# Kernel optimization log

Measured on AMD Instinct MI355X. Metric: run time of the kernel, lower is better.

Reference implementation:

```python
import jax, jax.numpy as jnp
import numpy as np

NUM_HEADS = 16


def setup_inputs() -> dict:
    key = jax.random.key(0)
    ks = jax.random.split(key, 8)
    B, S, D = 2, 2048, 1024
    q = jax.random.normal(ks[0], (B, S, D), dtype=jnp.float32)
    k = jax.random.normal(ks[1], (B, S, D), dtype=jnp.float32)
    v = jax.random.normal(ks[2], (B, S, D), dtype=jnp.float32)
    mask = jax.random.randint(ks[3], (1, 1, S, S), 0, 2, dtype=jnp.int32)
    sc = 1.0 / np.sqrt(D)
    wq = jax.random.normal(ks[4], (D, D), dtype=jnp.float32) * sc
    wk = jax.random.normal(ks[5], (D, D), dtype=jnp.float32) * sc
    wv = jax.random.normal(ks[6], (D, D), dtype=jnp.float32) * sc
    wout = jax.random.normal(ks[7], (D, D), dtype=jnp.float32) * sc
    return {"q": q, "k": k, "v": v, "mask": mask,
            "wq": wq, "wk": wk, "wv": wv, "wout": wout}


def reference(q, k, v, mask, wq, wk, wv, wout):
    B, S, D = q.shape
    H = NUM_HEADS
    hd = D // H

    def proj(x, w):
        # nn.Linear(bias=False): x @ w.T, then split heads -> [B,H,S,hd]
        return (x @ w.T).reshape(B, -1, H, hd).transpose(0, 2, 1, 3)

    qh, kh, vh = proj(q, wq), proj(k, wk), proj(v, wv)
    scale = jnp.asarray(hd, q.dtype) ** 0.5
    scores = jnp.einsum('bhqd,bhkd->bhqk', qh, kh) / scale  # [B,H,S,S]
    att = jax.nn.softmax(scores, axis=-1)
    # NOTE: original applies masked_fill AFTER softmax with value -1e-9
    att = jnp.where(mask == 0, jnp.asarray(-1e-9, att.dtype), att)
    out = jnp.einsum('bhqk,bhkd->bhqd', att, vh)  # [B,H,S,hd]
    out = out.transpose(0, 2, 1, 3).reshape(B, S, D)
    return out @ wout.T
```

## Files before the change

### kernel.cpp

```cpp
#include <hip/hip_runtime.h>
#include <stdint.h>


#define BATCH  2
#define S_LEN  2048
#define DMODEL 1024
#define NH     16
#define HD     64

typedef __bf16 bf16_t;
typedef short  short8 __attribute__((ext_vector_type(8)));
typedef float  f32x4  __attribute__((ext_vector_type(4)));

#define AS1 __attribute__((address_space(1)))
#define AS3 __attribute__((address_space(3)))

static constexpr size_t MB = (size_t)1 << 20;
static constexpr size_t WS_REQUIRED = 112 * MB;
#define OFF_XHI(z)  ((size_t)(z) * 16 * MB)
#define OFF_XLO(z)  (OFF_XHI(z) + 8 * MB)
#define OFF_WHI(z)  (48 * MB + (size_t)(z) * 4 * MB)
#define OFF_WLO(z)  (OFF_WHI(z) + 2 * MB)
#define OFF_PHI(z)  (64 * MB + (size_t)(z) * 16 * MB)
#define OFF_PLO(z)  (OFF_PHI(z) + 8 * MB)
#define OFF_OHI     ((size_t)0)
#define OFF_OLO     (8 * MB)
#define OFF_MASKB   (16 * MB)

__device__ __forceinline__ f32x4 mfma_bf16(short8 a, short8 b, f32x4 c) {
    return __builtin_amdgcn_mfma_f32_16x16x32_bf16(a, b, c, 0, 0, 0);
}

__device__ __forceinline__ short8 ld8(const bf16_t* p) {
    return *reinterpret_cast<const short8*>(p);
}

__global__ void cvt_split_kernel(const float* __restrict__ x,
                                 bf16_t* __restrict__ hi, bf16_t* __restrict__ lo,
                                 int n) {
    int i = (blockIdx.x * blockDim.x + threadIdx.x) * 4;
    if (i >= n) return;
    const float4 v = *reinterpret_cast<const float4*>(x + i);
    float s[4] = {v.x, v.y, v.z, v.w};
    ushort hbits[4], lbits[4];
#pragma unroll
    for (int j = 0; j < 4; j++) {
        bf16_t hh = (bf16_t)s[j];
        bf16_t ll = (bf16_t)(s[j] - (float)hh);
        hbits[j] = __builtin_bit_cast(ushort, hh);
        lbits[j] = __builtin_bit_cast(ushort, ll);
    }
    *reinterpret_cast<ushort4*>(hi + i) = ushort4{hbits[0], hbits[1], hbits[2], hbits[3]};
    *reinterpret_cast<ushort4*>(lo + i) = ushort4{lbits[0], lbits[1], lbits[2], lbits[3]};
}

__global__ void cvt_mask_kernel(const int* __restrict__ m, bf16_t* __restrict__ mb, int n) {
    int i = (blockIdx.x * blockDim.x + threadIdx.x) * 4;
    if (i >= n) return;
    const int4 v = *reinterpret_cast<const int4*>(m + i);
    int s[4] = {v.x, v.y, v.z, v.w};
    ushort b[4];
#pragma unroll
    for (int j = 0; j < 4; j++) {
        bf16_t t = (bf16_t)(s[j] ? 1.0f : 0.0f);
        b[j] = __builtin_bit_cast(ushort, t);
    }
    *reinterpret_cast<ushort4*>(mb + i) = ushort4{b[0], b[1], b[2], b[3]};
}

template <int FINAL>
__global__ __launch_bounds__(256, 2) void gemm_split_kernel(char* __restrict__ ws,
                                                            float* __restrict__ fout) {
    __shared__ __align__(16) bf16_t As[128 * 32];
    __shared__ __align__(16) bf16_t Bs[128 * 32];

    const int z = FINAL ? 3 : blockIdx.z;
    const bf16_t* Ahi = FINAL ? (const bf16_t*)(ws + OFF_OHI) : (const bf16_t*)(ws + OFF_XHI(z));
    const bf16_t* Alo = FINAL ? (const bf16_t*)(ws + OFF_OLO) : (const bf16_t*)(ws + OFF_XLO(z));
    const bf16_t* Bhi = (const bf16_t*)(ws + OFF_WHI(z));
    const bf16_t* Blo = (const bf16_t*)(ws + OFF_WLO(z));
    bf16_t* Ohi = FINAL ? nullptr : (bf16_t*)(ws + OFF_PHI(z));
    bf16_t* Olo = FINAL ? nullptr : (bf16_t*)(ws + OFF_PLO(z));
    const float scale = (!FINAL && z == 0) ? 0.125f : 1.0f;

    const int tid = threadIdx.x;
    const int lane = tid & 63, w = tid >> 6;
    const int wr = w >> 1, wc = w & 1;
    const int fr = lane & 15, fg = lane >> 4;
    const int m0 = blockIdx.x * 128, n0 = blockIdx.y * 128;
    const int K = 1024;

    const bf16_t* Aseg[3] = {Ahi, Ahi, Alo};
    const bf16_t* Bseg[3] = {Bhi, Blo, Bhi};

    f32x4 acc[4][4];
#pragma unroll
    for (int i = 0; i < 4; i++)
#pragma unroll
        for (int j = 0; j < 4; j++) acc[i][j] = f32x4{0.f, 0.f, 0.f, 0.f};

    AS3 bf16_t* asA = (AS3 bf16_t*)As;
    AS3 bf16_t* asB = (AS3 bf16_t*)Bs;

#pragma unroll 1
    for (int seg = 0; seg < 3; ++seg) {
        const bf16_t* Ab = Aseg[seg];
        const bf16_t* Bb = Bseg[seg];
#pragma unroll 1
        for (int ks = 0; ks < K; ks += 32) {
            __syncthreads();
#pragma unroll
            for (int i = 0; i < 2; i++) {
                const int c = i * 256 + tid;
                const int row = c >> 2;
                const int ce = (c & 3) * 8;
                __builtin_amdgcn_global_load_lds((const AS1 void*)(Ab + (size_t)(m0 + row) * K + ks + ce),
                                                 (AS3 void*)(asA + (size_t)(i * 256 + w * 64) * 8),
                                                 16, 0, 0);
                __builtin_amdgcn_global_load_lds((const AS1 void*)(Bb + (size_t)(n0 + row) * K + ks + ce),
                                                 (AS3 void*)(asB + (size_t)(i * 256 + w * 64) * 8),
                                                 16, 0, 0);
            }
            __syncthreads();

            short8 af[4], bfr[4];
#pragma unroll
            for (int i = 0; i < 4; i++) {
                af[i]  = ld8(&As[(wr * 64 + i * 16 + fr) * 32 + fg * 8]);
                bfr[i] = ld8(&Bs[(wc * 64 + i * 16 + fr) * 32 + fg * 8]);
            }
#pragma unroll
            for (int i = 0; i < 4; i++)
#pragma unroll
                for (int j = 0; j < 4; j++)
                    acc[i][j] = mfma_bf16(af[i], bfr[j], acc[i][j]);
        }
    }

#pragma unroll
    for (int i = 0; i < 4; i++) {
#pragma unroll
        for (int j = 0; j < 4; j++) {
            const int ncol = n0 + wc * 64 + j * 16 + fr;
#pragma unroll
            for (int r = 0; r < 4; r++) {
                const int m = m0 + wr * 64 + i * 16 + fg * 4 + r;
                const float val = acc[i][j][r] * scale;
                if (FINAL) {
                    fout[(size_t)m * DMODEL + ncol] = val;
                } else {
                    const bf16_t h = (bf16_t)val;
                    const bf16_t l = (bf16_t)(val - (float)h);
                    const int b = m >> 11, s = m & (S_LEN - 1);
                    const int hh = ncol >> 6, d = ncol & (HD - 1);
                    size_t idx;
                    if (z == 2) idx = ((size_t)(b * NH + hh) * HD + d) * S_LEN + s;
                    else        idx = ((size_t)(b * NH + hh) * S_LEN + s) * HD + d;
                    Ohi[idx] = h;
                    Olo[idx] = l;
                }
            }
        }
    }
}

__global__ __launch_bounds__(256, 2) void attn_kernel(char* __restrict__ ws) {
    __shared__ __align__(16) bf16_t KsH[8 * 64 * 8];
    __shared__ __align__(16) bf16_t KsL[8 * 64 * 8];
    __shared__ __align__(16) bf16_t VsH[8 * 64 * 8];
    __shared__ __align__(16) bf16_t VsL[8 * 64 * 8];

    const bf16_t* Qhi = (const bf16_t*)(ws + OFF_PHI(0));
    const bf16_t* Qlo = (const bf16_t*)(ws + OFF_PLO(0));
    const bf16_t* Khi = (const bf16_t*)(ws + OFF_PHI(1));
    const bf16_t* Klo = (const bf16_t*)(ws + OFF_PLO(1));
    const bf16_t* Vhi = (const bf16_t*)(ws + OFF_PHI(2));
    const bf16_t* Vlo = (const bf16_t*)(ws + OFF_PLO(2));
    const bf16_t* Mb  = (const bf16_t*)(ws + OFF_MASKB);
    bf16_t* Ohi = (bf16_t*)(ws + OFF_OHI);
    bf16_t* Olo = (bf16_t*)(ws + OFF_OLO);

    const int tid = threadIdx.x, lane = tid & 63, w = tid >> 6;
    const int fr = lane & 15, fg = lane >> 4;
    const int bh = blockIdx.y;
    const int q0 = blockIdx.x * 64;
    const int qrow = q0 + w * 16 + fr;
    const size_t qkBase = (size_t)bh * S_LEN * HD;
    const size_t vtBase = (size_t)bh * HD * S_LEN;

    size_t kSrc[2], vSrc[2];
#pragma unroll
    for (int i = 0; i < 2; i++) {
        const int s = i * 256 + tid;
        const int l = s & 63, f = (s >> 6) & 7;
        const int sfr = l & 15, sfg = l >> 4;
        const int cf = f >> 1, kc = f & 1;
        const int r = (cf & 1) * 4 + (sfr & 3) + (sfr >> 2) * 8 + (cf >> 1) * 32;
        kSrc[i] = qkBase + (size_t)r * HD + kc * 32 + sfg * 8;
        vSrc[i] = vtBase + (size_t)((f >> 1) * 16 + sfr) * S_LEN + (f & 1) * 32 + sfg * 8;
    }

    AS3 bf16_t* asKH = (AS3 bf16_t*)KsH;
    AS3 bf16_t* asKL = (AS3 bf16_t*)KsL;
    AS3 bf16_t* asVH = (AS3 bf16_t*)VsH;
    AS3 bf16_t* asVL = (AS3 bf16_t*)VsL;

    short8 qh[2], ql[2];
#pragma unroll
    for (int kc = 0; kc < 2; kc++) {
        const size_t off = qkBase + (size_t)qrow * HD + kc * 32 + fg * 8;
        qh[kc] = ld8(Qhi + off);
        ql[kc] = ld8(Qlo + off);
    }

    f32x4 acco[4];
#pragma unroll
    for (int df = 0; df < 4; df++) acco[df] = f32x4{0.f, 0.f, 0.f, 0.f};
    float mrun = -__builtin_inff(), lrun = 0.f;

    const size_t mrowBase = (size_t)qrow * S_LEN;

#pragma unroll 1
    for (int k0 = 0; k0 < S_LEN; k0 += 64) {
        __syncthreads();
#pragma unroll
        for (int i = 0; i < 2; i++) {
            const size_t ko = kSrc[i] + (size_t)k0 * HD;
            const size_t vo = vSrc[i] + k0;
            const size_t dst = (size_t)(i * 256 + w * 64) * 8;
            __builtin_amdgcn_global_load_lds((const AS1 void*)(Khi + ko), (AS3 void*)(asKH + dst), 16, 0, 0);
            __builtin_amdgcn_global_load_lds((const AS1 void*)(Klo + ko), (AS3 void*)(asKL + dst), 16, 0, 0);
            __builtin_amdgcn_global_load_lds((const AS1 void*)(Vhi + vo), (AS3 void*)(asVH + dst), 16, 0, 0);
            __builtin_amdgcn_global_load_lds((const AS1 void*)(Vlo + vo), (AS3 void*)(asVL + dst), 16, 0, 0);
        }
        const short8 mv0 = ld8(Mb + mrowBase + k0 + fg * 8);
        const short8 mv1 = ld8(Mb + mrowBase + k0 + 32 + fg * 8);
        __syncthreads();

        f32x4 sacc[4];
#pragma unroll
        for (int cf = 0; cf < 4; cf++) sacc[cf] = f32x4{0.f, 0.f, 0.f, 0.f};
#pragma unroll
        for (int cf = 0; cf < 4; cf++) {
#pragma unroll
            for (int kc = 0; kc < 2; kc++) {
                const int fi = cf * 2 + kc;
                const short8 kh = ld8(&KsH[(fi * 64 + lane) * 8]);
                const short8 kl = ld8(&KsL[(fi * 64 + lane) * 8]);
                sacc[cf] = mfma_bf16(kh, qh[kc], sacc[cf]);
                sacc[cf] = mfma_bf16(kl, qh[kc], sacc[cf]);
                sacc[cf] = mfma_bf16(kh, ql[kc], sacc[cf]);
            }
        }

        float mx = sacc[0][0];
#pragma unroll
        for (int cf = 0; cf < 4; cf++)
#pragma unroll
            for (int r = 0; r < 4; r++) mx = fmaxf(mx, sacc[cf][r]);
        mx = fmaxf(mx, __shfl_xor(mx, 16, 64));
        mx = fmaxf(mx, __shfl_xor(mx, 32, 64));
        const float mnew = fmaxf(mrun, mx);
        const float alpha = __expf(mrun - mnew);
        mrun = mnew;

        float p[4][4], psum = 0.f;
#pragma unroll
        for (int cf = 0; cf < 4; cf++)
#pragma unroll
            for (int r = 0; r < 4; r++) {
                p[cf][r] = __expf(sacc[cf][r] - mnew);
                psum += p[cf][r];
            }
        psum += __shfl_xor(psum, 16, 64);
        psum += __shfl_xor(psum, 32, 64);
        lrun = lrun * alpha + psum;
#pragma unroll
        for (int df = 0; df < 4; df++) acco[df] *= alpha;

        short8 phi[2], plo[2];
#pragma unroll
        for (int kc2 = 0; kc2 < 2; kc2++) {
#pragma unroll
            for (int j = 0; j < 8; j++) {
                const int cf = kc2 * 2 + (j >> 2), r = j & 3;
                const float mvf = (float)__builtin_bit_cast(
                    bf16_t, (ushort)((cf >> 1) ? mv1[(cf & 1) * 4 + r] : mv0[(cf & 1) * 4 + r]));
                const float pm = p[cf][r] * mvf;
                const bf16_t h = (bf16_t)pm;
                const bf16_t l = (bf16_t)(pm - (float)h);
                phi[kc2][j] = __builtin_bit_cast(short, h);
                plo[kc2][j] = __builtin_bit_cast(short, l);
            }
        }

#pragma unroll
        for (int kc2 = 0; kc2 < 2; kc2++) {
#pragma unroll
            for (int df = 0; df < 4; df++) {
                const int fi = df * 2 + kc2;
                const short8 vh = ld8(&VsH[(fi * 64 + lane) * 8]);
                const short8 vl = ld8(&VsL[(fi * 64 + lane) * 8]);
                acco[df] = mfma_bf16(vh, phi[kc2], acco[df]);
                acco[df] = mfma_bf16(vl, phi[kc2], acco[df]);
                acco[df] = mfma_bf16(vh, plo[kc2], acco[df]);
            }
        }
    }

    const int b = bh >> 4, hh = bh & (NH - 1);
    const float inv = 1.0f / lrun;
    const size_t obase = ((size_t)b * S_LEN + qrow) * DMODEL + hh * HD;
#pragma unroll
    for (int df = 0; df < 4; df++) {
#pragma unroll
        for (int r = 0; r < 4; r++) {
            const int d = df * 16 + fg * 4 + r;
            const float o = acco[df][r] * inv;
            const bf16_t h = (bf16_t)o;
            Ohi[obase + d] = h;
            Olo[obase + d] = (bf16_t)(o - (float)h);
        }
    }
}

extern "C" void kernel_launch(void* const* d_in, const int* in_sizes, int n_in,
                              void* d_out, int out_size, void* d_ws, size_t ws_size,
                              hipStream_t stream) {
    (void)in_sizes; (void)n_in; (void)out_size;
    if (ws_size < WS_REQUIRED) return;

    const float* q    = (const float*)d_in[0];
    const float* k    = (const float*)d_in[1];
    const float* v    = (const float*)d_in[2];
    const int*   mask = (const int*)  d_in[3];
    const float* wq   = (const float*)d_in[4];
    const float* wk   = (const float*)d_in[5];
    const float* wv   = (const float*)d_in[6];
    const float* wout = (const float*)d_in[7];
    char* ws = (char*)d_ws;
    float* out = (float*)d_out;

    const size_t nX = (size_t)BATCH * S_LEN * DMODEL;
    const size_t nW = (size_t)DMODEL * DMODEL;
    const size_t nM = (size_t)S_LEN * S_LEN;
    const dim3 blk(256);

    cvt_split_kernel<<<dim3(nX / 1024), blk, 0, stream>>>(q, (bf16_t*)(ws + OFF_XHI(0)), (bf16_t*)(ws + OFF_XLO(0)), (int)nX);
    cvt_split_kernel<<<dim3(nX / 1024), blk, 0, stream>>>(k, (bf16_t*)(ws + OFF_XHI(1)), (bf16_t*)(ws + OFF_XLO(1)), (int)nX);
    cvt_split_kernel<<<dim3(nX / 1024), blk, 0, stream>>>(v, (bf16_t*)(ws + OFF_XHI(2)), (bf16_t*)(ws + OFF_XLO(2)), (int)nX);
    cvt_split_kernel<<<dim3(nW / 1024), blk, 0, stream>>>(wq,   (bf16_t*)(ws + OFF_WHI(0)), (bf16_t*)(ws + OFF_WLO(0)), (int)nW);
    cvt_split_kernel<<<dim3(nW / 1024), blk, 0, stream>>>(wk,   (bf16_t*)(ws + OFF_WHI(1)), (bf16_t*)(ws + OFF_WLO(1)), (int)nW);
    cvt_split_kernel<<<dim3(nW / 1024), blk, 0, stream>>>(wv,   (bf16_t*)(ws + OFF_WHI(2)), (bf16_t*)(ws + OFF_WLO(2)), (int)nW);
    cvt_split_kernel<<<dim3(nW / 1024), blk, 0, stream>>>(wout, (bf16_t*)(ws + OFF_WHI(3)), (bf16_t*)(ws + OFF_WLO(3)), (int)nW);

    gemm_split_kernel<0><<<dim3(32, 8, 3), blk, 0, stream>>>(ws, nullptr);

    cvt_mask_kernel<<<dim3(nM / 1024), blk, 0, stream>>>(mask, (bf16_t*)(ws + OFF_MASKB), (int)nM);

    attn_kernel<<<dim3(S_LEN / 64, BATCH * NH), blk, 0, stream>>>(ws);

    gemm_split_kernel<1><<<dim3(32, 8, 1), blk, 0, stream>>>(ws, out);
}
```

Measured before the change: 485.6 us.

## Double-buffer attention K/V tiles and fuse split-bf16 GEMM segments

The attention kernel now double-buffers the K/V hi/lo tiles in LDS. It issues the next tile's async global-to-LDS loads and the next mask loads before computing on the current tile, with one barrier per iteration and s_setprio raised around the MFMA sections. The projection GEMM loads hi and lo tiles of both operands together and does all three split products in a single K loop, where it used to make three separate passes over K. This is meant to hide memory latency in attention and cut GEMM loop and barrier overhead and A/B reloads. The cost is double the LDS in both kernels, which may lower occupancy, plus more registers for the extra fragments.

```diff
diff --git a/kernel.cpp b/kernel.cpp
--- a/kernel.cpp
+++ b/kernel.cpp
@@ -71,8 +71,10 @@
 template <int FINAL>
 __global__ __launch_bounds__(256, 2) void gemm_split_kernel(char* __restrict__ ws,
                                                             float* __restrict__ fout) {
-    __shared__ __align__(16) bf16_t As[128 * 32];
-    __shared__ __align__(16) bf16_t Bs[128 * 32];
+    __shared__ __align__(16) bf16_t AsH[128 * 32];
+    __shared__ __align__(16) bf16_t AsL[128 * 32];
+    __shared__ __align__(16) bf16_t BsH[128 * 32];
+    __shared__ __align__(16) bf16_t BsL[128 * 32];
 
     const int z = FINAL ? 3 : blockIdx.z;
     const bf16_t* Ahi = FINAL ? (const bf16_t*)(ws + OFF_OHI) : (const bf16_t*)(ws + OFF_XHI(z));
@@ -90,51 +92,53 @@
     const int m0 = blockIdx.x * 128, n0 = blockIdx.y * 128;
     const int K = 1024;
 
-    const bf16_t* Aseg[3] = {Ahi, Ahi, Alo};
-    const bf16_t* Bseg[3] = {Bhi, Blo, Bhi};
-
     f32x4 acc[4][4];
 #pragma unroll
     for (int i = 0; i < 4; i++)
 #pragma unroll
         for (int j = 0; j < 4; j++) acc[i][j] = f32x4{0.f, 0.f, 0.f, 0.f};
 
-    AS3 bf16_t* asA = (AS3 bf16_t*)As;
-    AS3 bf16_t* asB = (AS3 bf16_t*)Bs;
+    AS3 bf16_t* asAH = (AS3 bf16_t*)AsH;
+    AS3 bf16_t* asAL = (AS3 bf16_t*)AsL;
+    AS3 bf16_t* asBH = (AS3 bf16_t*)BsH;
+    AS3 bf16_t* asBL = (AS3 bf16_t*)BsL;
 
 #pragma unroll 1
-    for (int seg = 0; seg < 3; ++seg) {
-        const bf16_t* Ab = Aseg[seg];
-        const bf16_t* Bb = Bseg[seg];
-#pragma unroll 1
-        for (int ks = 0; ks < K; ks += 32) {
-            __syncthreads();
-#pragma unroll
-            for (int i = 0; i < 2; i++) {
-                const int c = i * 256 + tid;
-                const int row = c >> 2;
-                const int ce = (c & 3) * 8;
-                __builtin_amdgcn_global_load_lds((const AS1 void*)(Ab + (size_t)(m0 + row) * K + ks + ce),
-                                                 (AS3 void*)(asA + (size_t)(i * 256 + w * 64) * 8),
-                                                 16, 0, 0);
-                __builtin_amdgcn_global_load_lds((const AS1 void*)(Bb + (size_t)(n0 + row) * K + ks + ce),
-                                                 (AS3 void*)(asB + (size_t)(i * 256 + w * 64) * 8),
-                                                 16, 0, 0);
-            }
-            __syncthreads();
-
-            short8 af[4], bfr[4];
-#pragma unroll
-            for (int i = 0; i < 4; i++) {
-                af[i]  = ld8(&As[(wr * 64 + i * 16 + fr) * 32 + fg * 8]);
-                bfr[i] = ld8(&Bs[(wc * 64 + i * 16 + fr) * 32 + fg * 8]);
-            }
-#pragma unroll
-            for (int i = 0; i < 4; i++)
-#pragma unroll
-                for (int j = 0; j < 4; j++)
-                    acc[i][j] = mfma_bf16(af[i], bfr[j], acc[i][j]);
-        }
+    for (int ks = 0; ks < K; ks += 32) {
+        __syncthreads();
+#pragma unroll
+        for (int i = 0; i < 2; i++) {
+            const int c = i * 256 + tid;
+            const int row = c >> 2;
+            const int ce = (c & 3) * 8;
+            const size_t gA = (size_t)(m0 + row) * K + ks + ce;
+            const size_t gB = (size_t)(n0 + row) * K + ks + ce;
+            const size_t d = (size_t)(i * 256 + w * 64) * 8;
+            __builtin_amdgcn_global_load_lds((const AS1 void*)(Ahi + gA), (AS3 void*)(asAH + d), 16, 0, 0);
+            __builtin_amdgcn_global_load_lds((const AS1 void*)(Alo + gA), (AS3 void*)(asAL + d), 16, 0, 0);
+            __builtin_amdgcn_global_load_lds((const AS1 void*)(Bhi + gB), (AS3 void*)(asBH + d), 16, 0, 0);
+            __builtin_amdgcn_global_load_lds((const AS1 void*)(Blo + gB), (AS3 void*)(asBL + d), 16, 0, 0);
+        }
+        __syncthreads();
+
+        short8 afh[4], afl[4], bfh[4], bfl[4];
+#pragma unroll
+        for (int i = 0; i < 4; i++) {
+            const int ao = (wr * 64 + i * 16 + fr) * 32 + fg * 8;
+            const int bo = (wc * 64 + i * 16 + fr) * 32 + fg * 8;
+            afh[i] = ld8(&AsH[ao]);
+            afl[i] = ld8(&AsL[ao]);
+            bfh[i] = ld8(&BsH[bo]);
+            bfl[i] = ld8(&BsL[bo]);
+        }
+#pragma unroll
+        for (int i = 0; i < 4; i++)
+#pragma unroll
+            for (int j = 0; j < 4; j++) {
+                acc[i][j] = mfma_bf16(afh[i], bfh[j], acc[i][j]);
+                acc[i][j] = mfma_bf16(afh[i], bfl[j], acc[i][j]);
+                acc[i][j] = mfma_bf16(afl[i], bfh[j], acc[i][j]);
+            }
     }
 
 #pragma unroll
@@ -165,10 +169,10 @@
 }
 
 __global__ __launch_bounds__(256, 2) void attn_kernel(char* __restrict__ ws) {
-    __shared__ __align__(16) bf16_t KsH[8 * 64 * 8];
-    __shared__ __align__(16) bf16_t KsL[8 * 64 * 8];
-    __shared__ __align__(16) bf16_t VsH[8 * 64 * 8];
-    __shared__ __align__(16) bf16_t VsL[8 * 64 * 8];
+    __shared__ __align__(16) bf16_t KsH[2][8 * 64 * 8];
+    __shared__ __align__(16) bf16_t KsL[2][8 * 64 * 8];
+    __shared__ __align__(16) bf16_t VsH[2][8 * 64 * 8];
+    __shared__ __align__(16) bf16_t VsL[2][8 * 64 * 8];
 
     const bf16_t* Qhi = (const bf16_t*)(ws + OFF_PHI(0));
     const bf16_t* Qlo = (const bf16_t*)(ws + OFF_PLO(0));
@@ -200,11 +204,6 @@
         vSrc[i] = vtBase + (size_t)((f >> 1) * 16 + sfr) * S_LEN + (f & 1) * 32 + sfg * 8;
     }
 
-    AS3 bf16_t* asKH = (AS3 bf16_t*)KsH;
-    AS3 bf16_t* asKL = (AS3 bf16_t*)KsL;
-    AS3 bf16_t* asVH = (AS3 bf16_t*)VsH;
-    AS3 bf16_t* asVL = (AS3 bf16_t*)VsL;
-
     short8 qh[2], ql[2];
 #pragma unroll
     for (int kc = 0; kc < 2; kc++) {
@@ -220,38 +219,55 @@
 
     const size_t mrowBase = (size_t)qrow * S_LEN;
 
+#define STAGE(K0, BUF)                                                                             \
+    {                                                                                              \
+        _Pragma("unroll") for (int i = 0; i < 2; i++) {                                            \
+            const size_t ko = kSrc[i] + (size_t)(K0) * HD;                                         \
+            const size_t vo = vSrc[i] + (K0);                                                      \
+            const size_t dst = (size_t)(i * 256 + w * 64) * 8;                                     \
+            __builtin_amdgcn_global_load_lds((const AS1 void*)(Khi + ko),                          \
+                                             (AS3 void*)((AS3 bf16_t*)KsH[BUF] + dst), 16, 0, 0);  \
+            __builtin_amdgcn_global_load_lds((const AS1 void*)(Klo + ko),                          \
+                                             (AS3 void*)((AS3 bf16_t*)KsL[BUF] + dst), 16, 0, 0);  \
+            __builtin_amdgcn_global_load_lds((const AS1 void*)(Vhi + vo),                          \
+                                             (AS3 void*)((AS3 bf16_t*)VsH[BUF] + dst), 16, 0, 0);  \
+            __builtin_amdgcn_global_load_lds((const AS1 void*)(Vlo + vo),                          \
+                                             (AS3 void*)((AS3 bf16_t*)VsL[BUF] + dst), 16, 0, 0);  \
+        }                                                                                          \
+    }
+
+    STAGE(0, 0)
+    short8 mv0Cur = ld8(Mb + mrowBase + fg * 8);
+    short8 mv1Cur = ld8(Mb + mrowBase + 32 + fg * 8);
+    short8 mv0Nxt = mv0Cur, mv1Nxt = mv1Cur;
+    __syncthreads();
+
+    int cur = 0;
 #pragma unroll 1
     for (int k0 = 0; k0 < S_LEN; k0 += 64) {
-        __syncthreads();
-#pragma unroll
-        for (int i = 0; i < 2; i++) {
-            const size_t ko = kSrc[i] + (size_t)k0 * HD;
-            const size_t vo = vSrc[i] + k0;
-            const size_t dst = (size_t)(i * 256 + w * 64) * 8;
-            __builtin_amdgcn_global_load_lds((const AS1 void*)(Khi + ko), (AS3 void*)(asKH + dst), 16, 0, 0);
-            __builtin_amdgcn_global_load_lds((const AS1 void*)(Klo + ko), (AS3 void*)(asKL + dst), 16, 0, 0);
-            __builtin_amdgcn_global_load_lds((const AS1 void*)(Vhi + vo), (AS3 void*)(asVH + dst), 16, 0, 0);
-            __builtin_amdgcn_global_load_lds((const AS1 void*)(Vlo + vo), (AS3 void*)(asVL + dst), 16, 0, 0);
-        }
-        const short8 mv0 = ld8(Mb + mrowBase + k0 + fg * 8);
-        const short8 mv1 = ld8(Mb + mrowBase + k0 + 32 + fg * 8);
-        __syncthreads();
+        if (k0 + 64 < S_LEN) {
+            STAGE(k0 + 64, cur ^ 1)
+            mv0Nxt = ld8(Mb + mrowBase + (k0 + 64) + fg * 8);
+            mv1Nxt = ld8(Mb + mrowBase + (k0 + 64) + 32 + fg * 8);
+        }
 
         f32x4 sacc[4];
 #pragma unroll
         for (int cf = 0; cf < 4; cf++) sacc[cf] = f32x4{0.f, 0.f, 0.f, 0.f};
+        __builtin_amdgcn_s_setprio(1);
 #pragma unroll
         for (int cf = 0; cf < 4; cf++) {
 #pragma unroll
             for (int kc = 0; kc < 2; kc++) {
                 const int fi = cf * 2 + kc;
-                const short8 kh = ld8(&KsH[(fi * 64 + lane) * 8]);
-                const short8 kl = ld8(&KsL[(fi * 64 + lane) * 8]);
+                const short8 kh = ld8(&KsH[cur][(fi * 64 + lane) * 8]);
+                const short8 kl = ld8(&KsL[cur][(fi * 64 + lane) * 8]);
                 sacc[cf] = mfma_bf16(kh, qh[kc], sacc[cf]);
                 sacc[cf] = mfma_bf16(kl, qh[kc], sacc[cf]);
                 sacc[cf] = mfma_bf16(kh, ql[kc], sacc[cf]);
             }
         }
+        __builtin_amdgcn_s_setprio(0);
 
         float mx = sacc[0][0];
 #pragma unroll
@@ -285,7 +301,7 @@
             for (int j = 0; j < 8; j++) {
                 const int cf = kc2 * 2 + (j >> 2), r = j & 3;
                 const float mvf = (float)__builtin_bit_cast(
-                    bf16_t, (ushort)((cf >> 1) ? mv1[(cf & 1) * 4 + r] : mv0[(cf & 1) * 4 + r]));
+                    bf16_t, (ushort)((cf >> 1) ? mv1Cur[(cf & 1) * 4 + r] : mv0Cur[(cf & 1) * 4 + r]));
                 const float pm = p[cf][r] * mvf;
                 const bf16_t h = (bf16_t)pm;
                 const bf16_t l = (bf16_t)(pm - (float)h);
@@ -294,19 +310,27 @@
             }
         }
 
+        __builtin_amdgcn_s_setprio(1);
 #pragma unroll
         for (int kc2 = 0; kc2 < 2; kc2++) {
 #pragma unroll
             for (int df = 0; df < 4; df++) {
                 const int fi = df * 2 + kc2;
-                const short8 vh = ld8(&VsH[(fi * 64 + lane) * 8]);
-                const short8 vl = ld8(&VsL[(fi * 64 + lane) * 8]);
+                const short8 vh = ld8(&VsH[cur][(fi * 64 + lane) * 8]);
+                const short8 vl = ld8(&VsL[cur][(fi * 64 + lane) * 8]);
                 acco[df] = mfma_bf16(vh, phi[kc2], acco[df]);
                 acco[df] = mfma_bf16(vl, phi[kc2], acco[df]);
                 acco[df] = mfma_bf16(vh, plo[kc2], acco[df]);
             }
         }
-    }
+        __builtin_amdgcn_s_setprio(0);
+
+        __syncthreads();
+        mv0Cur = mv0Nxt;
+        mv1Cur = mv1Nxt;
+        cur ^= 1;
+    }
+#undef STAGE
 
     const int b = bh >> 4, hh = bh & (NH - 1);
     const float inv = 1.0f / lrun;
```

Result: faster. 441.7 us (-9.0%).
